# Performance work log

Hardware: AMD Instinct MI355X
Metric: run time of the kernel (lower is better)

Reference implementation:

```python
import jax, jax.numpy as jnp
import numpy as np

B, S, E, H, D = 4, 2048, 1024, 16, 64  # batch, seq, embed, heads, head_dim


def setup_inputs() -> dict:
    key = jax.random.key(0)
    k1, k2, k3 = jax.random.split(key, 3)
    x = jax.random.normal(k1, (B, S, E), dtype=jnp.float32)
    qkv_w = jax.random.normal(k2, (E, H, 3 * D), dtype=jnp.float32) * (1.0 / np.sqrt(E))
    qkv_b = jnp.zeros((H, 3 * D), dtype=jnp.float32)
    out_w = jax.random.normal(k3, (H, D, E), dtype=jnp.float32) * (1.0 / np.sqrt(H * D))
    out_b = jnp.zeros((E,), dtype=jnp.float32)
    return {"x": x, "qkv_w": qkv_w, "qkv_b": qkv_b, "out_w": out_w, "out_b": out_b}


def _large_negative_number(dtype):
    return jnp.asarray(-0.7 * jnp.finfo(dtype).max, dtype=dtype)


def reference(x, qkv_w, qkv_b, out_w, out_b):
    # qkv projection: LinearGeneral(E -> (H, 3D))
    qkv = jnp.einsum('bse,ehd->bshd', x, qkv_w) + qkv_b  # [B,S,H,3D]
    q, k, v = jnp.split(qkv, 3, axis=-1)  # each [B,S,H,D]
    logits = jnp.einsum('bqhd,bkhd->bhqk', q, k)  # [B,H,S,S]
    logits = logits / jnp.sqrt(jnp.asarray(q.shape[-1], logits.dtype))
    mask = jnp.tril(jnp.ones((q.shape[1], q.shape[1]), dtype=jnp.bool_))
    logits = jnp.where(mask, logits, _large_negative_number(logits.dtype))
    probs = jax.nn.softmax(logits, axis=-1)
    attn = jnp.einsum('bhqk,bkhd->bqhd', probs, v)  # [B,S,H,D]
    # output projection: LinearGeneral((H, D) -> E)
    return jnp.einsum('bqhd,hde->bqe', attn, out_w) + out_b
```

## Files before the change

kernel.cpp:

```cpp
#include <hip/hip_runtime.h>

typedef unsigned int u32;
typedef _Float16 f16;
typedef _Float16 f16x8 __attribute__((ext_vector_type(8)));
typedef _Float16 f16x4 __attribute__((ext_vector_type(4)));
typedef float f32x4 __attribute__((ext_vector_type(4)));

#define LOG2E 1.4426950408889634f

__device__ __forceinline__ void gl_lds16(const void* g, void* l) {
  __builtin_amdgcn_global_load_lds(
      (const __attribute__((address_space(1))) u32*)g,
      (__attribute__((address_space(3))) u32*)l, 16, 0, 0);
}

__device__ __forceinline__ f32x4 mfma16(f16x8 a, f16x8 b, f32x4 c) {
  return __builtin_amdgcn_mfma_f32_16x16x32_f16(a, b, c, 0, 0, 0);
}

__global__ void k_cvt(const float* __restrict__ in, f16* __restrict__ out, int n4) {
  int stride = gridDim.x * blockDim.x;
  for (int i = blockIdx.x * blockDim.x + threadIdx.x; i < n4; i += stride) {
    f32x4 v = *(const f32x4*)(in + (size_t)i * 4);
    f16x4 o;
    o[0] = (f16)v[0]; o[1] = (f16)v[1]; o[2] = (f16)v[2]; o[3] = (f16)v[3];
    *(f16x4*)(out + (size_t)i * 4) = o;
  }
}

__global__ void k_tconv(const float* __restrict__ in, f16* __restrict__ out, int R, int C) {
  __shared__ f16 tile[32][33];
  int c0 = blockIdx.x * 32, r0 = blockIdx.y * 32;
  int tx = threadIdx.x, ty = threadIdx.y;
#pragma unroll
  for (int i = ty; i < 32; i += 8)
    tile[i][tx] = (f16)in[(size_t)(r0 + i) * C + c0 + tx];
  __syncthreads();
#pragma unroll
  for (int i = ty; i < 32; i += 8)
    out[(size_t)(c0 + i) * R + r0 + tx] = tile[tx][i];
}


__global__ __launch_bounds__(512, 4) void k_gemm_qkv2(
    const f16* __restrict__ A, const f16* __restrict__ Bt,
    const float* __restrict__ bias,
    f16* __restrict__ qo, f16* __restrict__ ko2, f16* __restrict__ vto) {
  constexpr int NT = 32;
  __shared__ __align__(16) f16 As[3 * 128 * 32];
  __shared__ __align__(16) f16 Bs[3 * 256 * 32];
  const int bn = blockIdx.x * 256, bm = blockIdx.y * 128;
  const int t = threadIdx.x, lane = t & 63, w = t >> 6;
  const int wr = w >> 2, wc = w & 3;
  const int g = lane >> 4, rl = lane & 15;
  const int lr = lane >> 2, lp = lane & 3;

  const int arow = w * 16 + lr;
  const f16* aSrc = A + (size_t)(bm + arow) * 1024 + (lp ^ ((arow >> 1) & 3)) * 8;
  const int brow0 = w * 32 + lr, brow1 = brow0 + 16;
  const f16* bSrc0 = Bt + (size_t)(bn + brow0) * 1024 + (lp ^ ((brow0 >> 1) & 3)) * 8;
  const f16* bSrc1 = Bt + (size_t)(bn + brow1) * 1024 + (lp ^ ((brow1 >> 1) & 3)) * 8;
  f16* aDst = As + w * 512;
  f16* bDst0 = Bs + w * 1024;
  f16* bDst1 = bDst0 + 512;

  f32x4 acc[4][4] = {};

  gl_lds16(aSrc, aDst);
  gl_lds16(bSrc0, bDst0);
  gl_lds16(bSrc1, bDst1);
  gl_lds16(aSrc + 32, aDst + 4096);
  gl_lds16(bSrc0 + 32, bDst0 + 8192);
  gl_lds16(bSrc1 + 32, bDst1 + 8192);

  int c = 0, cs = 2;
#pragma unroll 1
  for (int kt = 0; kt < NT; ++kt) {
    if (kt + 1 < NT) { asm volatile("s_waitcnt vmcnt(3)" ::: "memory"); }
    else             { asm volatile("s_waitcnt vmcnt(0)" ::: "memory"); }
    __builtin_amdgcn_sched_barrier(0);
    __builtin_amdgcn_s_barrier();
    __builtin_amdgcn_sched_barrier(0);

    if (kt + 2 < NT) {
      const int ko = (kt + 2) * 32;
      gl_lds16(aSrc + ko, aDst + cs * 4096);
      gl_lds16(bSrc0 + ko, bDst0 + cs * 8192);
      gl_lds16(bSrc1 + ko, bDst1 + cs * 8192);
    }

    const f16* Ab = As + c * 4096;
    const f16* Bb = Bs + c * 8192;
    f16x8 af[4], bf[4];
#pragma unroll
    for (int i = 0; i < 4; ++i) {
      const int r = wr * 64 + i * 16 + rl;
      af[i] = *(const f16x8*)(Ab + r * 32 + ((g ^ ((r >> 1) & 3)) * 8));
    }
#pragma unroll
    for (int j = 0; j < 4; ++j) {
      const int rb = wc * 64 + j * 16 + rl;
      bf[j] = *(const f16x8*)(Bb + rb * 32 + ((g ^ ((rb >> 1) & 3)) * 8));
    }
    __builtin_amdgcn_s_setprio(1);
#pragma unroll
    for (int i = 0; i < 4; ++i)
#pragma unroll
      for (int j = 0; j < 4; ++j)
        acc[i][j] = mfma16(af[i], bf[j], acc[i][j]);
    __builtin_amdgcn_s_setprio(0);
    __builtin_amdgcn_sched_barrier(0);

    c = (c == 2) ? 0 : c + 1;
    cs = (cs == 2) ? 0 : cs + 1;
  }

#pragma unroll
  for (int i = 0; i < 4; ++i)
#pragma unroll
    for (int j = 0; j < 4; ++j)
#pragma unroll
      for (int r = 0; r < 4; ++r) {
        int m = bm + wr * 64 + i * 16 + g * 4 + r;
        int n = bn + wc * 64 + j * 16 + rl;
        float v = acc[i][j][r] + bias[n];
        int b = m >> 11, s = m & 2047;
        int h = n / 192, rem = n - h * 192;
        int tsel = rem >> 6, d = rem & 63;
        size_t bh = (size_t)(b * 16 + h);
        if (tsel == 0)      qo[(bh * 2048 + s) * 64 + d] = (f16)(v * (0.125f * LOG2E));
        else if (tsel == 1) ko2[(bh * 2048 + s) * 64 + d] = (f16)v;
        else                vto[(bh * 64 + d) * 2048 + s] = (f16)v;
      }
}

__global__ __launch_bounds__(512, 4) void k_gemm_out2(
    const f16* __restrict__ A, const f16* __restrict__ Bt,
    const float* __restrict__ bias, float* __restrict__ out) {
  constexpr int NT = 32;
  __shared__ __align__(16) f16 As[3 * 128 * 32];
  __shared__ __align__(16) f16 Bs[3 * 256 * 32];
  const int bn = blockIdx.x * 256, bm = blockIdx.y * 128;
  const int t = threadIdx.x, lane = t & 63, w = t >> 6;
  const int wr = w >> 2, wc = w & 3;
  const int g = lane >> 4, rl = lane & 15;
  const int lr = lane >> 2, lp = lane & 3;

  const int arow = w * 16 + lr;
  const f16* aSrc = A + (size_t)(bm + arow) * 1024 + (lp ^ ((arow >> 1) & 3)) * 8;
  const int brow0 = w * 32 + lr, brow1 = brow0 + 16;
  const f16* bSrc0 = Bt + (size_t)(bn + brow0) * 1024 + (lp ^ ((brow0 >> 1) & 3)) * 8;
  const f16* bSrc1 = Bt + (size_t)(bn + brow1) * 1024 + (lp ^ ((brow1 >> 1) & 3)) * 8;
  f16* aDst = As + w * 512;
  f16* bDst0 = Bs + w * 1024;
  f16* bDst1 = bDst0 + 512;

  f32x4 acc[4][4] = {};

  gl_lds16(aSrc, aDst);
  gl_lds16(bSrc0, bDst0);
  gl_lds16(bSrc1, bDst1);
  gl_lds16(aSrc + 32, aDst + 4096);
  gl_lds16(bSrc0 + 32, bDst0 + 8192);
  gl_lds16(bSrc1 + 32, bDst1 + 8192);

  int c = 0, cs = 2;
#pragma unroll 1
  for (int kt = 0; kt < NT; ++kt) {
    if (kt + 1 < NT) { asm volatile("s_waitcnt vmcnt(3)" ::: "memory"); }
    else             { asm volatile("s_waitcnt vmcnt(0)" ::: "memory"); }
    __builtin_amdgcn_sched_barrier(0);
    __builtin_amdgcn_s_barrier();
    __builtin_amdgcn_sched_barrier(0);

    if (kt + 2 < NT) {
      const int ko = (kt + 2) * 32;
      gl_lds16(aSrc + ko, aDst + cs * 4096);
      gl_lds16(bSrc0 + ko, bDst0 + cs * 8192);
      gl_lds16(bSrc1 + ko, bDst1 + cs * 8192);
    }

    const f16* Ab = As + c * 4096;
    const f16* Bb = Bs + c * 8192;
    f16x8 af[4], bf[4];
#pragma unroll
    for (int i = 0; i < 4; ++i) {
      const int r = wr * 64 + i * 16 + rl;
      af[i] = *(const f16x8*)(Ab + r * 32 + ((g ^ ((r >> 1) & 3)) * 8));
    }
#pragma unroll
    for (int j = 0; j < 4; ++j) {
      const int rb = wc * 64 + j * 16 + rl;
      bf[j] = *(const f16x8*)(Bb + rb * 32 + ((g ^ ((rb >> 1) & 3)) * 8));
    }
    __builtin_amdgcn_s_setprio(1);
#pragma unroll
    for (int i = 0; i < 4; ++i)
#pragma unroll
      for (int j = 0; j < 4; ++j)
        acc[i][j] = mfma16(af[i], bf[j], acc[i][j]);
    __builtin_amdgcn_s_setprio(0);
    __builtin_amdgcn_sched_barrier(0);

    c = (c == 2) ? 0 : c + 1;
    cs = (cs == 2) ? 0 : cs + 1;
  }

#pragma unroll
  for (int i = 0; i < 4; ++i)
#pragma unroll
    for (int j = 0; j < 4; ++j)
#pragma unroll
      for (int r = 0; r < 4; ++r) {
        int m = bm + wr * 64 + i * 16 + g * 4 + r;
        int n = bn + wc * 64 + j * 16 + rl;
        out[(size_t)m * 1024 + n] = acc[i][j][r] + bias[n];
      }
}

__global__ __launch_bounds__(256, 4) void k_attn2(
    const f16* __restrict__ q, const f16* __restrict__ kgl,
    const f16* __restrict__ vt, f16* __restrict__ o) {
  constexpr int S = 2048;
  __shared__ __align__(16) f16 Ks[2][64 * 64];
  __shared__ __align__(16) f16 Vs[2][64 * 64];
  __shared__ __align__(16) f16 Ps[4][16 * 64];

  const int blk = blockIdx.x;
  const int sidx = blk >> 3;
  const int bh = (blk & 7) * 8 + (sidx & 7);
  const int qb = 15 - (sidx >> 3);

  const int t = threadIdx.x, lane = t & 63, w = t >> 6;
  const int g = lane >> 4, rl = lane & 15;

  const f16* qp = q + ((size_t)bh * S + qb * 128) * 64;
  const f16* kb = kgl + (size_t)bh * S * 64;
  const f16* vb = vt + (size_t)bh * 64 * S;

  f16x8 qf[2][2];
#pragma unroll
  for (int sub = 0; sub < 2; ++sub)
#pragma unroll
    for (int ks = 0; ks < 2; ++ks)
      qf[sub][ks] = *(const f16x8*)(qp + (size_t)(w * 32 + sub * 16 + rl) * 64 + ks * 32 + g * 8);

  f32x4 oacc[2][4] = {};
  float lrow[2] = {0.f, 0.f};

  const int srow = lane >> 3;
  const int sslot = (lane & 7) ^ srow;

  const int nkt = 2 * qb + 2;
  const int qmaxw = qb * 128 + w * 32 + 31;

  auto STAGE = [&](int bufi, int kt) {
#pragma unroll
    for (int i = 0; i < 2; ++i) {
      const int r0 = w * 16 + i * 8;
      gl_lds16(kb + (size_t)(kt * 64 + r0 + srow) * 64 + sslot * 8, &Ks[bufi][r0 * 64]);
      gl_lds16(vb + (size_t)(r0 + srow) * S + kt * 64 + sslot * 8, &Vs[bufi][r0 * 64]);
    }
  };

  STAGE(0, 0);
  __syncthreads();
  int buf = 0;

  for (int kt = 0; kt < nkt; ++kt) {
    if (kt + 1 < nkt) STAGE(buf ^ 1, kt + 1);

    if (kt * 64 <= qmaxw) {
      const f16* Kb = &Ks[buf][0];
      const f16* Vb = &Vs[buf][0];
#pragma unroll
      for (int sub = 0; sub < 2; ++sub) {
        const int qsub = qb * 128 + w * 32 + sub * 16;
        if (kt * 64 > qsub + 15) continue;

        f32x4 sT[4] = {};
#pragma unroll
        for (int j = 0; j < 4; ++j)
#pragma unroll
          for (int ks = 0; ks < 2; ++ks) {
            int row = j * 16 + rl;
            f16x8 kf = *(const f16x8*)(Kb + row * 64 + (((ks * 4 + g) ^ (rl & 7)) * 8));
            sT[j] = mfma16(kf, qf[sub][ks], sT[j]);
          }

        if (kt * 64 + 63 > qsub) {
#pragma unroll
          for (int j = 0; j < 4; ++j)
#pragma unroll
            for (int r = 0; r < 4; ++r)
              if (kt * 64 + j * 16 + g * 4 + r > qsub + rl) sT[j][r] = -1e30f;
        }

        float ps = 0.f;
#pragma unroll
        for (int j = 0; j < 4; ++j) {
          f16x4 pb;
#pragma unroll
          for (int r = 0; r < 4; ++r) {
            float p = exp2f(sT[j][r]);
            ps += p;
            pb[r] = (f16)p;
          }
          *(f16x4*)(&Ps[w][0] + rl * 64 + (((j * 2 + (g >> 1)) ^ (rl & 7)) * 8) + (g & 1) * 4) = pb;
        }
        lrow[sub] += ps;

        asm volatile("s_waitcnt lgkmcnt(0)" ::: "memory");
        __builtin_amdgcn_sched_barrier(0);

        f16x8 pf[2];
#pragma unroll
        for (int ks = 0; ks < 2; ++ks)
          pf[ks] = *(const f16x8*)(&Ps[w][0] + rl * 64 + (((ks * 4 + g) ^ (rl & 7)) * 8));

#pragma unroll
        for (int dj = 0; dj < 4; ++dj)
#pragma unroll
          for (int ks = 0; ks < 2; ++ks) {
            int vrow = dj * 16 + rl;
            f16x8 vf = *(const f16x8*)(Vb + vrow * 64 + (((ks * 4 + g) ^ (rl & 7)) * 8));
            oacc[sub][dj] = mfma16(pf[ks], vf, oacc[sub][dj]);
          }
      }
    }
    __syncthreads();
    buf ^= 1;
  }

  float rinv[2];
#pragma unroll
  for (int sub = 0; sub < 2; ++sub) {
    float s_ = lrow[sub];
    s_ += __shfl_xor(s_, 16, 64);
    s_ += __shfl_xor(s_, 32, 64);
    rinv[sub] = 1.0f / s_;
  }

  const int h = bh & 15;
  const size_t rowb = (size_t)(bh >> 4) * 2048 + qb * 128 + w * 32;
#pragma unroll
  for (int sub = 0; sub < 2; ++sub)
#pragma unroll
    for (int r = 0; r < 4; ++r) {
      float ri = __shfl(rinv[sub], g * 4 + r, 64);
#pragma unroll
      for (int dj = 0; dj < 4; ++dj)
        o[(rowb + sub * 16 + g * 4 + r) * 1024 + h * 64 + dj * 16 + rl] =
            (f16)(oacc[sub][dj][r] * ri);
    }
}

extern "C" void kernel_launch(void* const* d_in, const int* in_sizes, int n_in,
                              void* d_out, int out_size, void* d_ws, size_t ws_size,
                              hipStream_t stream) {
  (void)in_sizes; (void)n_in; (void)out_size; (void)ws_size;
  const float* x    = (const float*)d_in[0];
  const float* wqkv = (const float*)d_in[1];
  const float* bqkv = (const float*)d_in[2];
  const float* wo   = (const float*)d_in[3];
  const float* bo   = (const float*)d_in[4];
  float* out = (float*)d_out;
  char* ws = (char*)d_ws;

  f16* xb    = (f16*)(ws + 0);
  f16* wqkvt = (f16*)(ws + 16777216);
  f16* wot   = (f16*)(ws + 23068672);
  f16* qws   = (f16*)(ws + 25165824);
  f16* kws   = (f16*)(ws + 41943040);
  f16* vtws  = (f16*)(ws + 58720256);
  f16* attnb = xb;

  k_cvt<<<2048, 256, 0, stream>>>(x, xb, 8388608 / 4);
  k_tconv<<<dim3(96, 32), dim3(32, 8), 0, stream>>>(wqkv, wqkvt, 1024, 3072);
  k_tconv<<<dim3(32, 32), dim3(32, 8), 0, stream>>>(wo, wot, 1024, 1024);
  k_gemm_qkv2<<<dim3(12, 64), 512, 0, stream>>>(xb, wqkvt, bqkv, qws, kws, vtws);
  k_attn2<<<1024, 256, 0, stream>>>(qws, kws, vtws, attnb);
  k_gemm_out2<<<dim3(4, 64), 512, 0, stream>>>(attnb, wot, bo, out);
}
```

Before: 204.4 us.

## Restructure projection GEMMs into shared 256x128 core with K64 staging and swizzle

Both projection GEMMs now share one core that computes a 256x128 tile (instead of 128x256) with 8 waves, each owning a 64x64 sub-tile. Each pipeline step stages a K=64 slab split into two halves, interleaved with two MFMA phases separated by barriers. A grid swizzle remaps block indices to improve L2 reuse of the A and B panels. The aim is fewer barriers per unit of K, better global-to-LDS overlap and more cache-friendly ordering. The cost is about 144 KB of LDS per block, which drops occupancy to one block per CU, and more barriers inside each step.

Measured after the change: 203.9 us. About the same (-0.2%).

```diff
diff --git a/kernel.cpp b/kernel.cpp
--- a/kernel.cpp
+++ b/kernel.cpp
@@ -42,78 +42,120 @@
 }
 
 
-__global__ __launch_bounds__(512, 4) void k_gemm_qkv2(
+__device__ __forceinline__ void gemm_core(
+    const f16* __restrict__ A, const f16* __restrict__ Bt,
+    int bm, int bn, f16* SM, int w, int lane, f32x4 (&acc)[4][4]) {
+  constexpr int KT = 16;
+  const int g = lane >> 4, rl = lane & 15;
+  const int l4 = lane >> 2, ls = lane & 3;
+  const int wr = w >> 1, wc = w & 1;
+
+  const int cr0 = w * 32 + l4, cr1 = cr0 + 16, br = w * 16 + l4;
+  const f16* aS0 = A + (size_t)(bm + cr0) * 1024 + ((ls ^ ((cr0 >> 1) & 3)) * 8);
+  const f16* aS1 = A + (size_t)(bm + cr1) * 1024 + ((ls ^ ((cr1 >> 1) & 3)) * 8);
+  const f16* bS  = Bt + (size_t)(bn + br) * 1024 + ((ls ^ ((br >> 1) & 3)) * 8);
+
+#define STG_A(b, ks, kt) do { \
+    gl_lds16(aS0 + (kt) * 64 + (ks) * 32, SM + (b) * 16384 + (ks) * 8192 + (w * 2 + 0) * 512); \
+    gl_lds16(aS1 + (kt) * 64 + (ks) * 32, SM + (b) * 16384 + (ks) * 8192 + (w * 2 + 1) * 512); } while (0)
+#define STG_B(b, ks, kt) \
+    gl_lds16(bS + (kt) * 64 + (ks) * 32, SM + 49152 + (b) * 8192 + (ks) * 4096 + w * 512)
+
+  STG_A(0, 0, 0); STG_B(0, 0, 0); STG_A(0, 1, 0); STG_B(0, 1, 0);
+  STG_A(1, 0, 1); STG_B(1, 0, 1); STG_A(1, 1, 1); STG_B(1, 1, 1);
+  asm volatile("s_waitcnt vmcnt(6)" ::: "memory");
+  __builtin_amdgcn_s_barrier();
+
+  int c = 0, cs = 2;
+#pragma unroll 1
+  for (int kt = 0; kt < KT; ++kt) {
+    const f16* Ab = SM + c * 16384;
+    const f16* Bb = SM + 49152 + c * 8192;
+    const bool stg = (kt + 2 < KT);
+    f16x8 bf[4][2];
+
+    {
+#pragma unroll
+      for (int j = 0; j < 4; ++j)
+#pragma unroll
+        for (int ks = 0; ks < 2; ++ks) {
+          const int rb = wc * 64 + j * 16 + rl;
+          bf[j][ks] = *(const f16x8*)(Bb + ks * 4096 + rb * 32 + ((g ^ ((rb >> 1) & 3)) * 8));
+        }
+      f16x8 af[2][2];
+#pragma unroll
+      for (int mi = 0; mi < 2; ++mi)
+#pragma unroll
+        for (int ks = 0; ks < 2; ++ks) {
+          const int ra = wr * 64 + mi * 16 + rl;
+          af[mi][ks] = *(const f16x8*)(Ab + ks * 8192 + ra * 32 + ((g ^ ((ra >> 1) & 3)) * 8));
+        }
+      if (stg) { STG_A(cs, 0, kt + 2); STG_B(cs, 0, kt + 2); }
+      __builtin_amdgcn_s_barrier();
+      asm volatile("s_waitcnt lgkmcnt(0)" ::: "memory");
+      __builtin_amdgcn_sched_barrier(0);
+      __builtin_amdgcn_s_setprio(1);
+#pragma unroll
+      for (int mi = 0; mi < 2; ++mi)
+#pragma unroll
+        for (int j = 0; j < 4; ++j) {
+          acc[mi][j] = mfma16(af[mi][0], bf[j][0], acc[mi][j]);
+          acc[mi][j] = mfma16(af[mi][1], bf[j][1], acc[mi][j]);
+        }
+      __builtin_amdgcn_s_setprio(0);
+      __builtin_amdgcn_sched_barrier(0);
+      __builtin_amdgcn_s_barrier();
+    }
+
+    {
+      f16x8 af[2][2];
+#pragma unroll
+      for (int mi = 0; mi < 2; ++mi)
+#pragma unroll
+        for (int ks = 0; ks < 2; ++ks) {
+          const int ra = wr * 64 + (2 + mi) * 16 + rl;
+          af[mi][ks] = *(const f16x8*)(Ab + ks * 8192 + ra * 32 + ((g ^ ((ra >> 1) & 3)) * 8));
+        }
+      if (stg) { STG_A(cs, 1, kt + 2); STG_B(cs, 1, kt + 2); }
+      __builtin_amdgcn_s_barrier();
+      asm volatile("s_waitcnt lgkmcnt(0)" ::: "memory");
+      __builtin_amdgcn_sched_barrier(0);
+      __builtin_amdgcn_s_setprio(1);
+#pragma unroll
+      for (int mi = 0; mi < 2; ++mi)
+#pragma unroll
+        for (int j = 0; j < 4; ++j) {
+          acc[2 + mi][j] = mfma16(af[mi][0], bf[j][0], acc[2 + mi][j]);
+          acc[2 + mi][j] = mfma16(af[mi][1], bf[j][1], acc[2 + mi][j]);
+        }
+      __builtin_amdgcn_s_setprio(0);
+      __builtin_amdgcn_sched_barrier(0);
+      if (kt + 2 < KT)      { asm volatile("s_waitcnt vmcnt(6)" ::: "memory"); }
+      else if (kt + 1 < KT) { asm volatile("s_waitcnt vmcnt(0)" ::: "memory"); }
+      __builtin_amdgcn_s_barrier();
+    }
+
+    c = (c == 2) ? 0 : c + 1;
+    cs = (cs == 2) ? 0 : cs + 1;
+  }
+#undef STG_A
+#undef STG_B
+}
+
+__global__ __launch_bounds__(512, 2) void k_gemm_qkv3(
     const f16* __restrict__ A, const f16* __restrict__ Bt,
     const float* __restrict__ bias,
     f16* __restrict__ qo, f16* __restrict__ ko2, f16* __restrict__ vto) {
-  constexpr int NT = 32;
-  __shared__ __align__(16) f16 As[3 * 128 * 32];
-  __shared__ __align__(16) f16 Bs[3 * 256 * 32];
-  const int bn = blockIdx.x * 256, bm = blockIdx.y * 128;
+  __shared__ __align__(16) f16 SM[73728];
+  const int lin0 = blockIdx.y * 24 + blockIdx.x;
+  const int lin = (lin0 & 7) * 96 + (lin0 >> 3);
+  const int bn = (lin % 24) * 128, bm = (lin / 24) * 256;
   const int t = threadIdx.x, lane = t & 63, w = t >> 6;
-  const int wr = w >> 2, wc = w & 3;
   const int g = lane >> 4, rl = lane & 15;
-  const int lr = lane >> 2, lp = lane & 3;
-
-  const int arow = w * 16 + lr;
-  const f16* aSrc = A + (size_t)(bm + arow) * 1024 + (lp ^ ((arow >> 1) & 3)) * 8;
-  const int brow0 = w * 32 + lr, brow1 = brow0 + 16;
-  const f16* bSrc0 = Bt + (size_t)(bn + brow0) * 1024 + (lp ^ ((brow0 >> 1) & 3)) * 8;
-  const f16* bSrc1 = Bt + (size_t)(bn + brow1) * 1024 + (lp ^ ((brow1 >> 1) & 3)) * 8;
-  f16* aDst = As + w * 512;
-  f16* bDst0 = Bs + w * 1024;
-  f16* bDst1 = bDst0 + 512;
+  const int wr = w >> 1, wc = w & 1;
 
   f32x4 acc[4][4] = {};
-
-  gl_lds16(aSrc, aDst);
-  gl_lds16(bSrc0, bDst0);
-  gl_lds16(bSrc1, bDst1);
-  gl_lds16(aSrc + 32, aDst + 4096);
-  gl_lds16(bSrc0 + 32, bDst0 + 8192);
-  gl_lds16(bSrc1 + 32, bDst1 + 8192);
-
-  int c = 0, cs = 2;
-#pragma unroll 1
-  for (int kt = 0; kt < NT; ++kt) {
-    if (kt + 1 < NT) { asm volatile("s_waitcnt vmcnt(3)" ::: "memory"); }
-    else             { asm volatile("s_waitcnt vmcnt(0)" ::: "memory"); }
-    __builtin_amdgcn_sched_barrier(0);
-    __builtin_amdgcn_s_barrier();
-    __builtin_amdgcn_sched_barrier(0);
-
-    if (kt + 2 < NT) {
-      const int ko = (kt + 2) * 32;
-      gl_lds16(aSrc + ko, aDst + cs * 4096);
-      gl_lds16(bSrc0 + ko, bDst0 + cs * 8192);
-      gl_lds16(bSrc1 + ko, bDst1 + cs * 8192);
-    }
-
-    const f16* Ab = As + c * 4096;
-    const f16* Bb = Bs + c * 8192;
-    f16x8 af[4], bf[4];
-#pragma unroll
-    for (int i = 0; i < 4; ++i) {
-      const int r = wr * 64 + i * 16 + rl;
-      af[i] = *(const f16x8*)(Ab + r * 32 + ((g ^ ((r >> 1) & 3)) * 8));
-    }
-#pragma unroll
-    for (int j = 0; j < 4; ++j) {
-      const int rb = wc * 64 + j * 16 + rl;
-      bf[j] = *(const f16x8*)(Bb + rb * 32 + ((g ^ ((rb >> 1) & 3)) * 8));
-    }
-    __builtin_amdgcn_s_setprio(1);
-#pragma unroll
-    for (int i = 0; i < 4; ++i)
-#pragma unroll
-      for (int j = 0; j < 4; ++j)
-        acc[i][j] = mfma16(af[i], bf[j], acc[i][j]);
-    __builtin_amdgcn_s_setprio(0);
-    __builtin_amdgcn_sched_barrier(0);
-
-    c = (c == 2) ? 0 : c + 1;
-    cs = (cs == 2) ? 0 : cs + 1;
-  }
+  gemm_core(A, Bt, bm, bn, SM, w, lane, acc);
 
 #pragma unroll
   for (int i = 0; i < 4; ++i)
@@ -134,77 +176,19 @@
       }
 }
 
-__global__ __launch_bounds__(512, 4) void k_gemm_out2(
+__global__ __launch_bounds__(512, 2) void k_gemm_out3(
     const f16* __restrict__ A, const f16* __restrict__ Bt,
     const float* __restrict__ bias, float* __restrict__ out) {
-  constexpr int NT = 32;
-  __shared__ __align__(16) f16 As[3 * 128 * 32];
-  __shared__ __align__(16) f16 Bs[3 * 256 * 32];
-  const int bn = blockIdx.x * 256, bm = blockIdx.y * 128;
+  __shared__ __align__(16) f16 SM[73728];
+  const int lin0 = blockIdx.y * 8 + blockIdx.x;
+  const int lin = (lin0 & 7) * 32 + (lin0 >> 3);
+  const int bn = (lin % 8) * 128, bm = (lin / 8) * 256;
   const int t = threadIdx.x, lane = t & 63, w = t >> 6;
-  const int wr = w >> 2, wc = w & 3;
   const int g = lane >> 4, rl = lane & 15;
-  const int lr = lane >> 2, lp = lane & 3;
-
-  const int arow = w * 16 + lr;
-  const f16* aSrc = A + (size_t)(bm + arow) * 1024 + (lp ^ ((arow >> 1) & 3)) * 8;
-  const int brow0 = w * 32 + lr, brow1 = brow0 + 16;
-  const f16* bSrc0 = Bt + (size_t)(bn + brow0) * 1024 + (lp ^ ((brow0 >> 1) & 3)) * 8;
-  const f16* bSrc1 = Bt + (size_t)(bn + brow1) * 1024 + (lp ^ ((brow1 >> 1) & 3)) * 8;
-  f16* aDst = As + w * 512;
-  f16* bDst0 = Bs + w * 1024;
-  f16* bDst1 = bDst0 + 512;
+  const int wr = w >> 1, wc = w & 1;
 
   f32x4 acc[4][4] = {};
-
-  gl_lds16(aSrc, aDst);
-  gl_lds16(bSrc0, bDst0);
-  gl_lds16(bSrc1, bDst1);
-  gl_lds16(aSrc + 32, aDst + 4096);
-  gl_lds16(bSrc0 + 32, bDst0 + 8192);
-  gl_lds16(bSrc1 + 32, bDst1 + 8192);
-
-  int c = 0, cs = 2;
-#pragma unroll 1
-  for (int kt = 0; kt < NT; ++kt) {
-    if (kt + 1 < NT) { asm volatile("s_waitcnt vmcnt(3)" ::: "memory"); }
-    else             { asm volatile("s_waitcnt vmcnt(0)" ::: "memory"); }
-    __builtin_amdgcn_sched_barrier(0);
-    __builtin_amdgcn_s_barrier();
-    __builtin_amdgcn_sched_barrier(0);
-
-    if (kt + 2 < NT) {
-      const int ko = (kt + 2) * 32;
-      gl_lds16(aSrc + ko, aDst + cs * 4096);
-      gl_lds16(bSrc0 + ko, bDst0 + cs * 8192);
-      gl_lds16(bSrc1 + ko, bDst1 + cs * 8192);
-    }
-
-    const f16* Ab = As + c * 4096;
-    const f16* Bb = Bs + c * 8192;
-    f16x8 af[4], bf[4];
-#pragma unroll
-    for (int i = 0; i < 4; ++i) {
-      const int r = wr * 64 + i * 16 + rl;
-      af[i] = *(const f16x8*)(Ab + r * 32 + ((g ^ ((r >> 1) & 3)) * 8));
-    }
-#pragma unroll
-    for (int j = 0; j < 4; ++j) {
-      const int rb = wc * 64 + j * 16 + rl;
-      bf[j] = *(const f16x8*)(Bb + rb * 32 + ((g ^ ((rb >> 1) & 3)) * 8));
-    }
-    __builtin_amdgcn_s_setprio(1);
-#pragma unroll
-    for (int i = 0; i < 4; ++i)
-#pragma unroll
-      for (int j = 0; j < 4; ++j)
-        acc[i][j] = mfma16(af[i], bf[j], acc[i][j]);
-    __builtin_amdgcn_s_setprio(0);
-    __builtin_amdgcn_sched_barrier(0);
-
-    c = (c == 2) ? 0 : c + 1;
-    cs = (cs == 2) ? 0 : cs + 1;
-  }
+  gemm_core(A, Bt, bm, bn, SM, w, lane, acc);
 
 #pragma unroll
   for (int i = 0; i < 4; ++i)
@@ -378,7 +362,7 @@
   k_cvt<<<2048, 256, 0, stream>>>(x, xb, 8388608 / 4);
   k_tconv<<<dim3(96, 32), dim3(32, 8), 0, stream>>>(wqkv, wqkvt, 1024, 3072);
   k_tconv<<<dim3(32, 32), dim3(32, 8), 0, stream>>>(wo, wot, 1024, 1024);
-  k_gemm_qkv2<<<dim3(12, 64), 512, 0, stream>>>(xb, wqkvt, bqkv, qws, kws, vtws);
+  k_gemm_qkv3<<<dim3(24, 32), 512, 0, stream>>>(xb, wqkvt, bqkv, qws, kws, vtws);
   k_attn2<<<1024, 256, 0, stream>>>(qws, kws, vtws, attnb);
-  k_gemm_out2<<<dim3(4, 64), 512, 0, stream>>>(attnb, wot, bo, out);
-}
+  k_gemm_out3<<<dim3(8, 32), 512, 0, stream>>>(attnb, wot, bo, out);
+}
```
